# Kernel optimization log

Measured on AMD Instinct MI355X. Metric: run time of the kernel, lower is better.

## Reference

```python
import jax, jax.numpy as jnp
import numpy as np

N_NODES = 50000
N_EDGES = 800000
DIM = 128
N_LAYERS = 5
BN_EPS = 1e-5


def setup_inputs() -> dict:
    key = jax.random.key(0)
    ks = jax.random.split(key, 8)
    x = jax.random.normal(ks[0], (N_NODES, DIM), dtype=jnp.float32)
    edge_index = jax.random.randint(ks[1], (2, N_EDGES), 0, N_NODES, dtype=jnp.int64)
    batch = jnp.sort(jax.random.randint(ks[2], (N_NODES,), 0, 64, dtype=jnp.int64))
    scale = 1.0 / np.sqrt(DIM)
    W1 = jax.random.normal(ks[3], (N_LAYERS, DIM, DIM), dtype=jnp.float32) * scale
    b1 = jnp.zeros((N_LAYERS, DIM), dtype=jnp.float32)
    W2 = jax.random.normal(ks[4], (N_LAYERS, DIM, DIM), dtype=jnp.float32) * scale
    b2 = jnp.zeros((N_LAYERS, DIM), dtype=jnp.float32)
    gamma = jnp.ones((N_LAYERS, DIM), dtype=jnp.float32)
    beta = jnp.zeros((N_LAYERS, DIM), dtype=jnp.float32)
    return {"x": x, "edge_index": edge_index, "batch": batch,
            "W1": W1, "b1": b1, "W2": W2, "b2": b2,
            "gamma": gamma, "beta": beta}


def _gin_layer(x, src, dst, w1, bb1, w2, bb2, g, b):
    # GINConv (eps=0): h_i = MLP(x_i + sum_{j->i} x_j)
    agg = jax.ops.segment_sum(x[src], dst, num_segments=N_NODES)  # [N, D]
    h = x + agg
    h = jnp.maximum(h @ w1 + bb1, 0.0) @ w2 + bb2  # 2-layer MLP
    h = jnp.maximum(h, 0.0)                        # outer ReLU
    # BatchNorm1d (training-mode batch stats, biased variance)
    mu = jnp.mean(h, axis=0)
    var = jnp.mean(jnp.square(h - mu), axis=0)
    return (h - mu) * jax.lax.rsqrt(var + BN_EPS) * g + b


def reference(x, edge_index, batch, W1, b1, W2, b2, gamma, beta):
    src, dst = edge_index[0], edge_index[1]
    xs = []
    h = x
    for i in range(N_LAYERS):
        h = _gin_layer(h, src, dst, W1[i], b1[i], W2[i], b2[i], gamma[i], beta[i])
        xs.append(h)
    return h, jnp.stack(xs)
```

## Files before the change

### kernel.cpp

```cpp
#include <hip/hip_runtime.h>

#define N_NODES 50000
#define DIM 128
#define N_LAYERS 5
#define BN_EPS 1e-5f

typedef __attribute__((ext_vector_type(8))) short short8;
typedef __attribute__((ext_vector_type(4))) float f32x4;

__device__ __forceinline__ float bf2f(unsigned int u16) {
    union { unsigned int i; float f; } c; c.i = u16 << 16; return c.f;
}
__device__ __forceinline__ unsigned short f2bf(float f) {
    union { float f; unsigned int i; } c; c.f = f;
    unsigned int v = c.i + 0x7FFFu + ((c.i >> 16) & 1u);
    return (unsigned short)(v >> 16);
}


__global__ void hist_kernel(const int* __restrict__ dst, int n_edges, int* __restrict__ counts) {
    int e = blockIdx.x * 256 + threadIdx.x;
    if (e < n_edges) atomicAdd(&counts[dst[e]], 1);
}

__global__ void scan_local(const int* __restrict__ counts, int n,
                           int* __restrict__ offsets, int* __restrict__ blocksums) {
    __shared__ int temp[256];
    int t = threadIdx.x;
    int i = blockIdx.x * 256 + t;
    int v = (i < n) ? counts[i] : 0;
    temp[t] = v;
    __syncthreads();
    for (int off = 1; off < 256; off <<= 1) {
        int add = (t >= off) ? temp[t - off] : 0;
        __syncthreads();
        temp[t] += add;
        __syncthreads();
    }
    if (i < n) offsets[i] = temp[t] - v;
    if (t == 255) blocksums[blockIdx.x] = temp[255];
}

__global__ void scan_block(int* __restrict__ blocksums, int nb) {
    __shared__ int temp[256];
    int t = threadIdx.x;
    int v = (t < nb) ? blocksums[t] : 0;
    temp[t] = v;
    __syncthreads();
    for (int off = 1; off < 256; off <<= 1) {
        int add = (t >= off) ? temp[t - off] : 0;
        __syncthreads();
        temp[t] += add;
        __syncthreads();
    }
    if (t < nb) blocksums[t] = temp[t] - v;
}

__global__ void scan_add(int* __restrict__ offsets, int* __restrict__ cursor,
                         const int* __restrict__ blocksums, int n, int n_edges) {
    int i = blockIdx.x * 256 + threadIdx.x;
    if (i < n) {
        int val = offsets[i] + blocksums[blockIdx.x];
        offsets[i] = val;
        cursor[i] = val;
    }
    if (i == 0) offsets[n] = n_edges;
}

__global__ void scatter_kernel(const int* __restrict__ src, const int* __restrict__ dst,
                               int n_edges, int* __restrict__ cursor, int* __restrict__ csr_src) {
    int e = blockIdx.x * 256 + threadIdx.x;
    if (e < n_edges) {
        int p = atomicAdd(&cursor[dst[e]], 1);
        csr_src[p] = src[e];
    }
}


__global__ void wpack_prep(const float* __restrict__ W1, const float* __restrict__ W2,
                           unsigned short* __restrict__ wp) {
    int idx = blockIdx.x * 256 + threadIdx.x;
    if (idx >= N_LAYERS * 2 * 16384) return;
    int j    = idx & 7;
    int lane = (idx >> 3) & 63;
    int nt   = (idx >> 9) & 7;
    int ks   = (idx >> 12) & 3;
    int mat  = (idx >> 14) & 1;
    int lay  = idx >> 15;
    int l15 = lane & 15, l4 = lane >> 4;
    int col = nt * 16 + l15;
    int kp = ks * 32 + l4 * 8 + j;
    int k = mat ? ((kp & 7) * 16 + (kp >> 3)) : kp;
    const float* W = mat ? W2 : W1;
    float w = W[((size_t)lay * 128 + k) * 128 + col];
    unsigned short hi = f2bf(w);
    unsigned short lo = f2bf(w - bf2f(hi));
    size_t base = (size_t)(lay * 2 + mat) * 32768;
    size_t inner = (size_t)((ks * 8 + nt) * 64 + lane) * 8 + j;
    wp[base + inner] = hi;
    wp[base + 16384 + inner] = lo;
}


__global__ void agg_kernel(const float* __restrict__ x, const int* __restrict__ csr_src,
                           const int* __restrict__ offsets,
                           unsigned int* __restrict__ h_hi_u, unsigned int* __restrict__ h_lo_u) {
    int wave = threadIdx.x >> 6;
    int l = threadIdx.x & 63;
    int node = blockIdx.x * 4 + wave;
    if (node >= N_NODES) return;
    int half = l >> 5;
    int d4 = l & 31;
    int beg = offsets[node], end = offsets[node + 1];
    const float4* x4 = (const float4*)x;

    float4 acc = make_float4(0.f, 0.f, 0.f, 0.f);
    if (half == 0) acc = x4[(size_t)node * 32 + d4];

    for (int e = beg; e < end; e += 16) {
        int s[8];
#pragma unroll
        for (int i = 0; i < 8; ++i) s[i] = csr_src[min(e + 2 * i + half, end - 1)];
        float4 v[8];
#pragma unroll
        for (int i = 0; i < 8; ++i) v[i] = x4[(size_t)s[i] * 32 + d4];
#pragma unroll
        for (int i = 0; i < 8; ++i) {
            float w = (e + 2 * i + half < end) ? 1.0f : 0.0f;
            acc.x = fmaf(v[i].x, w, acc.x);
            acc.y = fmaf(v[i].y, w, acc.y);
            acc.z = fmaf(v[i].z, w, acc.z);
            acc.w = fmaf(v[i].w, w, acc.w);
        }
    }

    acc.x += __shfl_xor(acc.x, 32);
    acc.y += __shfl_xor(acc.y, 32);
    acc.z += __shfl_xor(acc.z, 32);
    acc.w += __shfl_xor(acc.w, 32);

    unsigned short h0 = f2bf(acc.x), h1 = f2bf(acc.y);
    unsigned short h2 = f2bf(acc.z), h3 = f2bf(acc.w);
    if (half == 0) {
        uint2 hv;
        hv.x = (unsigned int)h0 | ((unsigned int)h1 << 16);
        hv.y = (unsigned int)h2 | ((unsigned int)h3 << 16);
        ((uint2*)h_hi_u)[(size_t)node * 32 + d4] = hv;
    } else {
        unsigned short l0 = f2bf(acc.x - bf2f(h0)), l1 = f2bf(acc.y - bf2f(h1));
        unsigned short l2 = f2bf(acc.z - bf2f(h2)), l3 = f2bf(acc.w - bf2f(h3));
        uint2 lv;
        lv.x = (unsigned int)l0 | ((unsigned int)l1 << 16);
        lv.y = (unsigned int)l2 | ((unsigned int)l3 << 16);
        ((uint2*)h_lo_u)[(size_t)node * 32 + d4] = lv;
    }
}

__global__ __launch_bounds__(128) void mlp_mfma(
        const unsigned short* __restrict__ h_hi, const unsigned short* __restrict__ h_lo,
        const short8* __restrict__ wp1, const float* __restrict__ b1,
        const short8* __restrict__ wp2, const float* __restrict__ b2,
        float* __restrict__ h_raw,
        float* __restrict__ part_s, float* __restrict__ part_q) {
    __shared__ unsigned short mid_hi[2][2][16][128];
    __shared__ unsigned short mid_lo[2][2][16][128];
    __shared__ float red_s[2][128], red_q[2][128];
    int t = threadIdx.x, wave = t >> 6, l = t & 63;
    int l15 = l & 15, l4 = l >> 4;
    int row_base = blockIdx.x * 64 + wave * 32;

    int r0 = row_base + l15, r1 = r0 + 16;
    int cr0 = min(r0, N_NODES - 1), cr1 = min(r1, N_NODES - 1);
    const short8* ah0p = (const short8*)(h_hi + (size_t)cr0 * 128);
    const short8* ah1p = (const short8*)(h_hi + (size_t)cr1 * 128);
    const short8* al0p = (const short8*)(h_lo + (size_t)cr0 * 128);
    const short8* al1p = (const short8*)(h_lo + (size_t)cr1 * 128);

    const short8* wp1l = wp1 + 2048;
    const short8* wp2l = wp2 + 2048;

    f32x4 acc[2][8];
#pragma unroll
    for (int m = 0; m < 2; ++m)
#pragma unroll
        for (int nt = 0; nt < 8; ++nt) acc[m][nt] = (f32x4)0.0f;

#pragma unroll
    for (int ks = 0; ks < 4; ++ks) {
        short8 ah0 = ah0p[ks * 4 + l4];
        short8 ah1 = ah1p[ks * 4 + l4];
        short8 al0 = al0p[ks * 4 + l4];
        short8 al1 = al1p[ks * 4 + l4];
#pragma unroll
        for (int nt = 0; nt < 8; ++nt) {
            short8 whi = wp1[(ks * 8 + nt) * 64 + l];
            short8 wlo = wp1l[(ks * 8 + nt) * 64 + l];
            acc[0][nt] = __builtin_amdgcn_mfma_f32_16x16x32_bf16(ah0, whi, acc[0][nt], 0, 0, 0);
            acc[0][nt] = __builtin_amdgcn_mfma_f32_16x16x32_bf16(al0, whi, acc[0][nt], 0, 0, 0);
            acc[0][nt] = __builtin_amdgcn_mfma_f32_16x16x32_bf16(ah0, wlo, acc[0][nt], 0, 0, 0);
            acc[1][nt] = __builtin_amdgcn_mfma_f32_16x16x32_bf16(ah1, whi, acc[1][nt], 0, 0, 0);
            acc[1][nt] = __builtin_amdgcn_mfma_f32_16x16x32_bf16(al1, whi, acc[1][nt], 0, 0, 0);
            acc[1][nt] = __builtin_amdgcn_mfma_f32_16x16x32_bf16(ah1, wlo, acc[1][nt], 0, 0, 0);
        }
    }

    float b1v[8];
#pragma unroll
    for (int nt = 0; nt < 8; ++nt) b1v[nt] = b1[nt * 16 + l15];

#pragma unroll
    for (int m = 0; m < 2; ++m) {
#pragma unroll
        for (int rr = 0; rr < 4; ++rr) {
            int row = l4 * 4 + rr;
            short8 ph, pl;
#pragma unroll
            for (int nt = 0; nt < 8; ++nt) {
                float v = fmaxf(acc[m][nt][rr] + b1v[nt], 0.0f);
                unsigned short hv = f2bf(v);
                ph[nt] = (short)hv;
                pl[nt] = (short)f2bf(v - bf2f(hv));
            }
            int off = (l15 * 16) ^ ((row & 7) << 4);
            *(short8*)((char*)&mid_hi[wave][m][row][0] + off) = ph;
            *(short8*)((char*)&mid_lo[wave][m][row][0] + off) = pl;
        }
    }
    __syncthreads();

    f32x4 acc2[2][8];
#pragma unroll
    for (int m = 0; m < 2; ++m)
#pragma unroll
        for (int nt = 0; nt < 8; ++nt) acc2[m][nt] = (f32x4)0.0f;

#pragma unroll
    for (int ks = 0; ks < 4; ++ks) {
        int off = (ks * 64 + l4 * 16) ^ ((l15 & 7) << 4);
        short8 ah0 = *(const short8*)((char*)&mid_hi[wave][0][l15][0] + off);
        short8 ah1 = *(const short8*)((char*)&mid_hi[wave][1][l15][0] + off);
        short8 al0 = *(const short8*)((char*)&mid_lo[wave][0][l15][0] + off);
        short8 al1 = *(const short8*)((char*)&mid_lo[wave][1][l15][0] + off);
#pragma unroll
        for (int nt = 0; nt < 8; ++nt) {
            short8 whi = wp2[(ks * 8 + nt) * 64 + l];
            short8 wlo = wp2l[(ks * 8 + nt) * 64 + l];
            acc2[0][nt] = __builtin_amdgcn_mfma_f32_16x16x32_bf16(ah0, whi, acc2[0][nt], 0, 0, 0);
            acc2[0][nt] = __builtin_amdgcn_mfma_f32_16x16x32_bf16(al0, whi, acc2[0][nt], 0, 0, 0);
            acc2[0][nt] = __builtin_amdgcn_mfma_f32_16x16x32_bf16(ah0, wlo, acc2[0][nt], 0, 0, 0);
            acc2[1][nt] = __builtin_amdgcn_mfma_f32_16x16x32_bf16(ah1, whi, acc2[1][nt], 0, 0, 0);
            acc2[1][nt] = __builtin_amdgcn_mfma_f32_16x16x32_bf16(al1, whi, acc2[1][nt], 0, 0, 0);
            acc2[1][nt] = __builtin_amdgcn_mfma_f32_16x16x32_bf16(ah1, wlo, acc2[1][nt], 0, 0, 0);
        }
    }

    float b2v[8];
#pragma unroll
    for (int nt = 0; nt < 8; ++nt) b2v[nt] = b2[nt * 16 + l15];

    float s[8], q[8];
#pragma unroll
    for (int nt = 0; nt < 8; ++nt) { s[nt] = 0.0f; q[nt] = 0.0f; }

#pragma unroll
    for (int m = 0; m < 2; ++m) {
#pragma unroll
        for (int rr = 0; rr < 4; ++rr) {
            int rg = row_base + m * 16 + l4 * 4 + rr;
            bool ok = rg < N_NODES;
#pragma unroll
            for (int nt = 0; nt < 8; ++nt) {
                float v = fmaxf(acc2[m][nt][rr] + b2v[nt], 0.0f);
                if (ok) {
                    h_raw[(size_t)rg * 128 + nt * 16 + l15] = v;
                    s[nt] += v;
                    q[nt] += v * v;
                }
            }
        }
    }
#pragma unroll
    for (int nt = 0; nt < 8; ++nt) {
        s[nt] += __shfl_xor(s[nt], 16); s[nt] += __shfl_xor(s[nt], 32);
        q[nt] += __shfl_xor(q[nt], 16); q[nt] += __shfl_xor(q[nt], 32);
    }
    if (l4 == 0) {
#pragma unroll
        for (int nt = 0; nt < 8; ++nt) {
            red_s[wave][nt * 16 + l15] = s[nt];
            red_q[wave][nt * 16 + l15] = q[nt];
        }
    }
    __syncthreads();
    if (t < 128) {
        part_s[blockIdx.x * 128 + t] = red_s[0][t] + red_s[1][t];
        part_q[blockIdx.x * 128 + t] = red_q[0][t] + red_q[1][t];
    }
}

__global__ __launch_bounds__(256) void bn_reduce(
        const float* __restrict__ part_s, const float* __restrict__ part_q,
        float* __restrict__ bn_sum, float* __restrict__ bn_sq, int nparts) {
    __shared__ float red[256];
    int c = blockIdx.x & 127;
    const float* src = (blockIdx.x >> 7) ? part_q : part_s;
    float* dst = (blockIdx.x >> 7) ? bn_sq : bn_sum;
    float a = 0.0f;
    for (int p = threadIdx.x; p < nparts; p += 256) a += src[p * 128 + c];
    red[threadIdx.x] = a;
    __syncthreads();
    for (int s = 128; s > 0; s >>= 1) {
        if (threadIdx.x < s) red[threadIdx.x] += red[threadIdx.x + s];
        __syncthreads();
    }
    if (threadIdx.x == 0) dst[c] = red[0];
}

__global__ void bn_apply(float* __restrict__ h,
                         const float* __restrict__ bn_sum, const float* __restrict__ bn_sq,
                         const float* __restrict__ gamma, const float* __restrict__ beta,
                         float4* __restrict__ dup) {
    int i4 = blockIdx.x * 256 + threadIdx.x;
    if (i4 >= N_NODES * DIM / 4) return;
    float4 v = ((const float4*)h)[i4];
    int c0 = (i4 & 31) * 4;
    const float invN = 1.0f / (float)N_NODES;
    float* vp = (float*)&v;
#pragma unroll
    for (int j = 0; j < 4; ++j) {
        int c = c0 + j;
        float mean = bn_sum[c] * invN;
        float var = fmaxf(bn_sq[c] * invN - mean * mean, 0.0f);
        float inv = rsqrtf(var + BN_EPS);
        vp[j] = (vp[j] - mean) * inv * gamma[c] + beta[c];
    }
    ((float4*)h)[i4] = v;
    if (dup) dup[i4] = v;
}


extern "C" void kernel_launch(void* const* d_in, const int* in_sizes, int n_in,
                              void* d_out, int out_size, void* d_ws, size_t ws_size,
                              hipStream_t stream) {
    const float* x     = (const float*)d_in[0];
    const int*   eidx  = (const int*)d_in[1];
    const float* W1    = (const float*)d_in[3];
    const float* b1    = (const float*)d_in[4];
    const float* W2    = (const float*)d_in[5];
    const float* b2    = (const float*)d_in[6];
    const float* gamma = (const float*)d_in[7];
    const float* beta  = (const float*)d_in[8];

    int n_edges = in_sizes[1] / 2;
    const int* src = eidx;
    const int* dst = eidx + n_edges;

    const int NBLK = (N_NODES + 63) / 64;

    int* counts    = (int*)d_ws;
    int* offsets   = counts + N_NODES;
    int* cursor    = offsets + N_NODES + 1;
    int* blocksums = cursor + N_NODES;
    int* csr_src   = blocksums + 256;
    float* part_s  = (float*)(csr_src + n_edges);
    float* part_q  = part_s + NBLK * 128;
    float* bn_sum  = part_q + NBLK * 128;
    float* bn_sq   = bn_sum + DIM;
    size_t wp_off = (((size_t)(bn_sq + DIM) - (size_t)d_ws) + 15) & ~(size_t)15;
    unsigned short* wp = (unsigned short*)((char*)d_ws + wp_off);

    float* out = (float*)d_out;
    unsigned int* h_hi_u = (unsigned int*)d_out;
    unsigned int* h_lo_u = h_hi_u + (size_t)N_NODES * 64;
    const unsigned short* h_hi = (const unsigned short*)h_hi_u;
    const unsigned short* h_lo = (const unsigned short*)h_lo_u;

    hipMemsetAsync(counts, 0, N_NODES * sizeof(int), stream);
    hist_kernel<<<(n_edges + 255) / 256, 256, 0, stream>>>(dst, n_edges, counts);
    int nb = (N_NODES + 255) / 256;
    scan_local<<<nb, 256, 0, stream>>>(counts, N_NODES, offsets, blocksums);
    scan_block<<<1, 256, 0, stream>>>(blocksums, nb);
    scan_add<<<nb, 256, 0, stream>>>(offsets, cursor, blocksums, N_NODES, n_edges);
    scatter_kernel<<<(n_edges + 255) / 256, 256, 0, stream>>>(src, dst, n_edges, cursor, csr_src);

    wpack_prep<<<(N_LAYERS * 2 * 16384 + 255) / 256, 256, 0, stream>>>(W1, W2, wp);

    const float* layer_in = x;
    for (int i = 0; i < N_LAYERS; ++i) {
        float* layer_out = out + (size_t)(1 + i) * N_NODES * DIM;
        agg_kernel<<<(N_NODES + 3) / 4, 256, 0, stream>>>(layer_in, csr_src, offsets,
                                                          h_hi_u, h_lo_u);
        mlp_mfma<<<NBLK, 128, 0, stream>>>(
            h_hi, h_lo,
            (const short8*)(wp + (size_t)(i * 2) * 32768), b1 + (size_t)i * DIM,
            (const short8*)(wp + (size_t)(i * 2 + 1) * 32768), b2 + (size_t)i * DIM,
            layer_out, part_s, part_q);
        bn_reduce<<<256, 256, 0, stream>>>(part_s, part_q, bn_sum, bn_sq, NBLK);
        bn_apply<<<(N_NODES * DIM / 4 + 255) / 256, 256, 0, stream>>>(
            layer_out, bn_sum, bn_sq, gamma + (size_t)i * DIM, beta + (size_t)i * DIM,
            (i == N_LAYERS - 1) ? (float4*)out : (float4*)nullptr);
        layer_in = layer_out;
    }
}
```

Before: 598.9 us.

## Gather bf16 copies of layer activations in aggregation for layers after the first

bn_apply now also writes a bf16 copy of each normalized layer output into workspace, and layers 2-5 gather neighbor features from that bf16 buffer with a new aggregation kernel that loads 16-byte chunks, eight neighbors per quarter-wave. This halves the bytes fetched in the edge gather, which is the dominant memory cost. In exchange, neighbor inputs are rounded to bf16 before summation, which loses precision relative to the fp32 gather followed by hi/lo split, and bn_apply gains an extra write.

```diff
diff --git a/kernel.cpp b/kernel.cpp
--- a/kernel.cpp
+++ b/kernel.cpp
@@ -156,6 +156,78 @@
     }
 }
 
+__global__ void agg_bf_kernel(const uint4* __restrict__ xbf4, const int* __restrict__ csr_src,
+                              const int* __restrict__ offsets,
+                              unsigned int* __restrict__ h_hi_u, unsigned int* __restrict__ h_lo_u) {
+    int wave = threadIdx.x >> 6;
+    int l = threadIdx.x & 63;
+    int node = blockIdx.x * 4 + wave;
+    if (node >= N_NODES) return;
+    int quarter = l >> 4;
+    int d = l & 15;
+    int beg = offsets[node], end = offsets[node + 1];
+
+    float a[8];
+#pragma unroll
+    for (int j = 0; j < 8; ++j) a[j] = 0.0f;
+    if (quarter == 0) {
+        uint4 u = xbf4[(size_t)node * 16 + d];
+        a[0] = bf2f(u.x & 0xFFFFu); a[1] = bf2f(u.x >> 16);
+        a[2] = bf2f(u.y & 0xFFFFu); a[3] = bf2f(u.y >> 16);
+        a[4] = bf2f(u.z & 0xFFFFu); a[5] = bf2f(u.z >> 16);
+        a[6] = bf2f(u.w & 0xFFFFu); a[7] = bf2f(u.w >> 16);
+    }
+
+    for (int e = beg; e < end; e += 32) {
+        int s[8];
+#pragma unroll
+        for (int i = 0; i < 8; ++i) s[i] = csr_src[min(e + 4 * i + quarter, end - 1)];
+        uint4 v[8];
+#pragma unroll
+        for (int i = 0; i < 8; ++i) v[i] = xbf4[(size_t)s[i] * 16 + d];
+#pragma unroll
+        for (int i = 0; i < 8; ++i) {
+            float w = (e + 4 * i + quarter < end) ? 1.0f : 0.0f;
+            a[0] = fmaf(bf2f(v[i].x & 0xFFFFu), w, a[0]);
+            a[1] = fmaf(bf2f(v[i].x >> 16),     w, a[1]);
+            a[2] = fmaf(bf2f(v[i].y & 0xFFFFu), w, a[2]);
+            a[3] = fmaf(bf2f(v[i].y >> 16),     w, a[3]);
+            a[4] = fmaf(bf2f(v[i].z & 0xFFFFu), w, a[4]);
+            a[5] = fmaf(bf2f(v[i].z >> 16),     w, a[5]);
+            a[6] = fmaf(bf2f(v[i].w & 0xFFFFu), w, a[6]);
+            a[7] = fmaf(bf2f(v[i].w >> 16),     w, a[7]);
+        }
+    }
+
+#pragma unroll
+    for (int j = 0; j < 8; ++j) {
+        a[j] += __shfl_xor(a[j], 16);
+        a[j] += __shfl_xor(a[j], 32);
+    }
+
+    unsigned short h[8];
+#pragma unroll
+    for (int j = 0; j < 8; ++j) h[j] = f2bf(a[j]);
+    if (quarter == 0) {
+        uint4 hv;
+        hv.x = (unsigned int)h[0] | ((unsigned int)h[1] << 16);
+        hv.y = (unsigned int)h[2] | ((unsigned int)h[3] << 16);
+        hv.z = (unsigned int)h[4] | ((unsigned int)h[5] << 16);
+        hv.w = (unsigned int)h[6] | ((unsigned int)h[7] << 16);
+        ((uint4*)h_hi_u)[(size_t)node * 16 + d] = hv;
+    } else if (quarter == 1) {
+        unsigned short lo[8];
+#pragma unroll
+        for (int j = 0; j < 8; ++j) lo[j] = f2bf(a[j] - bf2f(h[j]));
+        uint4 lv;
+        lv.x = (unsigned int)lo[0] | ((unsigned int)lo[1] << 16);
+        lv.y = (unsigned int)lo[2] | ((unsigned int)lo[3] << 16);
+        lv.z = (unsigned int)lo[4] | ((unsigned int)lo[5] << 16);
+        lv.w = (unsigned int)lo[6] | ((unsigned int)lo[7] << 16);
+        ((uint4*)h_lo_u)[(size_t)node * 16 + d] = lv;
+    }
+}
+
 __global__ __launch_bounds__(128) void mlp_mfma(
         const unsigned short* __restrict__ h_hi, const unsigned short* __restrict__ h_lo,
         const short8* __restrict__ wp1, const float* __restrict__ b1,
@@ -319,7 +391,7 @@
 __global__ void bn_apply(float* __restrict__ h,
                          const float* __restrict__ bn_sum, const float* __restrict__ bn_sq,
                          const float* __restrict__ gamma, const float* __restrict__ beta,
-                         float4* __restrict__ dup) {
+                         uint2* __restrict__ xbf_next, float4* __restrict__ dup) {
     int i4 = blockIdx.x * 256 + threadIdx.x;
     if (i4 >= N_NODES * DIM / 4) return;
     float4 v = ((const float4*)h)[i4];
@@ -335,6 +407,11 @@
         vp[j] = (vp[j] - mean) * inv * gamma[c] + beta[c];
     }
     ((float4*)h)[i4] = v;
+    if (xbf_next) {
+        unsigned int lo = (unsigned int)f2bf(vp[0]) | ((unsigned int)f2bf(vp[1]) << 16);
+        unsigned int hi = (unsigned int)f2bf(vp[2]) | ((unsigned int)f2bf(vp[3]) << 16);
+        xbf_next[i4] = make_uint2(lo, hi);
+    }
     if (dup) dup[i4] = v;
 }
 
@@ -368,6 +445,8 @@
     float* bn_sq   = bn_sum + DIM;
     size_t wp_off = (((size_t)(bn_sq + DIM) - (size_t)d_ws) + 15) & ~(size_t)15;
     unsigned short* wp = (unsigned short*)((char*)d_ws + wp_off);
+    size_t xb_off = (wp_off + (size_t)N_LAYERS * 2 * 32768 * 2 + 15) & ~(size_t)15;
+    uint2* x_bf2 = (uint2*)((char*)d_ws + xb_off);
 
     float* out = (float*)d_out;
     unsigned int* h_hi_u = (unsigned int*)d_out;
@@ -385,11 +464,15 @@
 
     wpack_prep<<<(N_LAYERS * 2 * 16384 + 255) / 256, 256, 0, stream>>>(W1, W2, wp);
 
-    const float* layer_in = x;
     for (int i = 0; i < N_LAYERS; ++i) {
         float* layer_out = out + (size_t)(1 + i) * N_NODES * DIM;
-        agg_kernel<<<(N_NODES + 3) / 4, 256, 0, stream>>>(layer_in, csr_src, offsets,
-                                                          h_hi_u, h_lo_u);
+        if (i == 0)
+            agg_kernel<<<(N_NODES + 3) / 4, 256, 0, stream>>>(x, csr_src, offsets,
+                                                              h_hi_u, h_lo_u);
+        else
+            agg_bf_kernel<<<(N_NODES + 3) / 4, 256, 0, stream>>>((const uint4*)x_bf2,
+                                                                 csr_src, offsets,
+                                                                 h_hi_u, h_lo_u);
         mlp_mfma<<<NBLK, 128, 0, stream>>>(
             h_hi, h_lo,
             (const short8*)(wp + (size_t)(i * 2) * 32768), b1 + (size_t)i * DIM,
@@ -398,7 +481,7 @@
         bn_reduce<<<256, 256, 0, stream>>>(part_s, part_q, bn_sum, bn_sq, NBLK);
         bn_apply<<<(N_NODES * DIM / 4 + 255) / 256, 256, 0, stream>>>(
             layer_out, bn_sum, bn_sq, gamma + (size_t)i * DIM, beta + (size_t)i * DIM,
+            (i < N_LAYERS - 1) ? x_bf2 : (uint2*)nullptr,
             (i == N_LAYERS - 1) ? (float4*)out : (float4*)nullptr);
-        layer_in = layer_out;
-    }
-}
+    }
+}
```

Measured after the change: 537.5 us. 1.11x faster.
